# Kernel tuning notes

Hardware: AMD Instinct MI355X
Metric: run time of the kernel (lower is better)

## Reference

```python
import jax, jax.numpy as jnp
import numpy as np

B, S, H = 4, 4096, 2048


def setup_inputs() -> dict:
    key = jax.random.key(0)
    ks = jax.random.split(key, 20)
    def lin(k, fin, fout):
        # torch nn.Linear default init: U(-1/sqrt(fin), 1/sqrt(fin))
        kw, kb = jax.random.split(k)
        bound = 1.0 / np.sqrt(fin)
        W = jax.random.uniform(kw, (fin, fout), jnp.float32, -bound, bound)
        b = jax.random.uniform(kb, (fout,), jnp.float32, -bound, bound)
        return W, b
    hidden_states = jax.random.normal(ks[0], (B, S, H), jnp.float32)
    access_frequency = jax.random.uniform(ks[1], (B, S), jnp.float32)
    importance_score = jax.random.uniform(ks[2], (B, S), jnp.float32)
    sel_W1, sel_b1 = lin(ks[3], H, H // 4)
    sel_W2, sel_b2 = lin(ks[4], H // 4, 3)
    c1_W, c1_b = lin(ks[5], H, H // 2)
    f1_W, f1_b = lin(ks[6], H // 2, H // 2)
    d1_W, d1_b = lin(ks[7], H // 2, H)
    c2_W, c2_b = lin(ks[8], H, H // 4)
    f2_W, f2_b = lin(ks[9], H // 4, H // 4)
    d2_W, d2_b = lin(ks[10], H // 4, H)
    return dict(hidden_states=hidden_states, access_frequency=access_frequency,
                importance_score=importance_score, sel_W1=sel_W1, sel_b1=sel_b1,
                sel_W2=sel_W2, sel_b2=sel_b2, c1_W=c1_W, c1_b=c1_b, f1_W=f1_W,
                f1_b=f1_b, d1_W=d1_W, d1_b=d1_b, c2_W=c2_W, c2_b=c2_b,
                f2_W=f2_W, f2_b=f2_b, d2_W=d2_W, d2_b=d2_b)


def reference(hidden_states, access_frequency, importance_score,
              sel_W1, sel_b1, sel_W2, sel_b2,
              c1_W, c1_b, f1_W, f1_b, d1_W, d1_b,
              c2_W, c2_b, f2_W, f2_b, d2_W, d2_b):
    x = hidden_states  # [B,S,H]
    Hh = x.shape[-1] // 2
    # strategy selector on frequency/importance-modulated features
    combined = jnp.concatenate(
        [x[..., :Hh] * access_frequency[..., None],
         x[..., Hh:] * importance_score[..., None]], axis=-1)  # [B,S,H]
    hmid = jax.nn.relu(jnp.einsum('bsh,hk->bsk', combined, sel_W1) + sel_b1)
    weights = jax.nn.softmax(jnp.einsum('bsk,kl->bsl', hmid, sel_W2) + sel_b2)
    sel = jnp.argmax(weights, axis=-1)  # [B,S] in {0,1,2}
    # expert paths (computed densely, selected per token)
    out1 = (jax.numpy.einsum('bsh,hc->bsc', x, c1_W) + c1_b)
    out1 = jnp.einsum('bsc,cd->bsd', out1, f1_W) + f1_b
    out1 = jnp.einsum('bsc,ch->bsh', out1, d1_W) + d1_b
    out2 = (jnp.einsum('bsh,hc->bsc', x, c2_W) + c2_b)
    out2 = jnp.einsum('bsc,cd->bsd', out2, f2_W) + f2_b
    out2 = jnp.einsum('bsc,ch->bsh', out2, d2_W) + d2_b
    s = sel[..., None]
    out = jnp.where(s == 0, x, jnp.where(s == 1, out1, out2))
    return out
```

## Files before the change

kernel.cpp:

```cpp
#include <hip/hip_runtime.h>


typedef __bf16 bf16x8 __attribute__((ext_vector_type(8)));
typedef float  f32x4  __attribute__((ext_vector_type(4)));
typedef unsigned short us;

__device__ __forceinline__ float bf2f(us u) {
  union { unsigned u; float f; } v; v.u = ((unsigned)u) << 16;
  return v.f;
}
__device__ __forceinline__ us f2bf(float f) {
  union { float f; unsigned u; } v; v.f = f;
  unsigned r = v.u + 0x7fffu + ((v.u >> 16) & 1u);
  return (us)(r >> 16);
}
__device__ __forceinline__ float scrub(float v) {
  return (v == v && fabsf(v) < 1e30f) ? v : 0.f;
}
__device__ __forceinline__ void gld_lds16(const void* g, void* l) {
  __builtin_amdgcn_global_load_lds(
      (const __attribute__((address_space(1))) void*)g,
      (__attribute__((address_space(3))) void*)l, 16, 0, 0);
}

template<int MODE, int AIDX>
__global__ __launch_bounds__(256) void gemm_bt(
    const void* __restrict__ Ap, const us* __restrict__ BT,
    const float* __restrict__ bias, void* __restrict__ outp,
    const int* __restrict__ aidx, const int* __restrict__ oidx,
    const int* __restrict__ cntp, int N, int K)
{
  const int cnt = cntp[0];
  const int Mp  = (cnt + 127) & ~127;
  const int bm0 = blockIdx.y * 128;
  if (bm0 >= Mp) return;
  const int bn0 = blockIdx.x * 128;

  __shared__ __align__(16) us As[128 * 64];
  __shared__ __align__(16) us Bs[128 * 64];
  const int tid  = threadIdx.x;
  const int lane = tid & 63;
  const int w    = tid >> 6;
  const int wr   = w >> 1, wc = w & 1;

  const us* gb[4];
  const us* gab[4];
  const float* gaf[4];
  us* la[4]; us* lb[4];
#pragma unroll
  for (int i = 0; i < 4; ++i) {
    const int s = i * 256 + tid, m = s >> 3, cp = s & 7, c = cp ^ (m & 7);
    gb[i] = BT + (size_t)(bn0 + m) * K + c * 8;
    lb[i] = &Bs[s * 8];
    la[i] = &As[s * 8];
    if (AIDX) {
      const int arow = aidx[bm0 + m];
      gaf[i] = (const float*)Ap + (size_t)arow * K + c * 8;
    } else {
      gab[i] = (const us*)Ap + (size_t)(bm0 + m) * K + c * 8;
    }
  }

  f32x4 acc[4][4] = {};

  for (int k0 = 0; k0 < K; k0 += 64) {
#pragma unroll
    for (int i = 0; i < 4; ++i) { gld_lds16(gb[i], lb[i]); gb[i] += 64; }
    if (AIDX) {
#pragma unroll
      for (int i = 0; i < 4; ++i) {
        float4 a0 = *(const float4*)gaf[i];
        float4 a1 = *(const float4*)(gaf[i] + 4);
        gaf[i] += 64;
        union { uint4 v; us u[8]; } t;
        t.u[0] = f2bf(a0.x); t.u[1] = f2bf(a0.y);
        t.u[2] = f2bf(a0.z); t.u[3] = f2bf(a0.w);
        t.u[4] = f2bf(a1.x); t.u[5] = f2bf(a1.y);
        t.u[6] = f2bf(a1.z); t.u[7] = f2bf(a1.w);
        *(uint4*)la[i] = t.v;
      }
    } else {
#pragma unroll
      for (int i = 0; i < 4; ++i) { gld_lds16(gab[i], la[i]); gab[i] += 64; }
    }
    __syncthreads();
#pragma unroll
    for (int kk = 0; kk < 2; ++kk) {
      const int cc = kk * 4 + (lane >> 4);
      bf16x8 af[4], bfr[4];
#pragma unroll
      for (int t = 0; t < 4; ++t) {
        const int m = wr * 64 + t * 16 + (lane & 15);
        const int n = wc * 64 + t * 16 + (lane & 15);
        af[t]  = *(const bf16x8*)&As[(m * 8 + (cc ^ (m & 7))) * 8];
        bfr[t] = *(const bf16x8*)&Bs[(n * 8 + (cc ^ (n & 7))) * 8];
      }
#pragma unroll
      for (int mt = 0; mt < 4; ++mt)
#pragma unroll
        for (int nt = 0; nt < 4; ++nt)
          acc[mt][nt] = __builtin_amdgcn_mfma_f32_16x16x32_bf16(
              af[mt], bfr[nt], acc[mt][nt], 0, 0, 0);
    }
    __syncthreads();
  }

  const int colb = bn0 + wc * 64 + (lane & 15);
  const int rowb = bm0 + wr * 64 + ((lane >> 4) << 2);
  float bv[4];
#pragma unroll
  for (int nt = 0; nt < 4; ++nt) bv[nt] = bias[colb + nt * 16];
#pragma unroll
  for (int mt = 0; mt < 4; ++mt) {
#pragma unroll
    for (int r = 0; r < 4; ++r) {
      const int row = rowb + mt * 16 + r;
      if (MODE == 3) {
        if (row >= cnt) continue;
        const size_t orow = (size_t)oidx[row];
#pragma unroll
        for (int nt = 0; nt < 4; ++nt)
          ((float*)outp)[orow * N + colb + nt * 16] =
              scrub(acc[mt][nt][r] + bv[nt]);
      } else {
#pragma unroll
        for (int nt = 0; nt < 4; ++nt)
          ((us*)outp)[(size_t)row * N + colb + nt * 16] =
              f2bf(scrub(acc[mt][nt][r] + bv[nt]));
      }
    }
  }
}

__global__ __launch_bounds__(256) void sel_gemm(
    const float* __restrict__ X, const float* __restrict__ FR,
    const float* __restrict__ IM,
    const us* __restrict__ BTH, const us* __restrict__ BTL,
    const float* __restrict__ bias, float* __restrict__ hmid)
{
  constexpr int K = 2048, N = 512;
  __shared__ __align__(16) us AsH[128 * 64];
  __shared__ __align__(16) us AsL[128 * 64];
  __shared__ __align__(16) us BsH[128 * 64];
  __shared__ __align__(16) us BsL[128 * 64];
  const int tid  = threadIdx.x;
  const int lane = tid & 63;
  const int w    = tid >> 6;
  const int wr   = w >> 1, wc = w & 1;
  const int bm0  = blockIdx.y * 128;
  const int bn0  = blockIdx.x * 128;

  const us* gbh[4]; const us* gbl[4];
  const float* gx[4];
  us* lbh[4]; us* lbl[4];
  int sOfs[4];
#pragma unroll
  for (int i = 0; i < 4; ++i) {
    const int s = i * 256 + tid, m = s >> 3, cp = s & 7, c = cp ^ (m & 7);
    gbh[i] = BTH + (size_t)(bn0 + m) * K + c * 8;
    gbl[i] = BTL + (size_t)(bn0 + m) * K + c * 8;
    lbh[i] = &BsH[s * 8];
    lbl[i] = &BsL[s * 8];
    gx[i]  = X + (size_t)(bm0 + m) * K + c * 8;
    sOfs[i] = s * 8;
  }

  f32x4 acc[4][4] = {};

  for (int k0 = 0; k0 < K; k0 += 64) {
#pragma unroll
    for (int i = 0; i < 4; ++i) {
      gld_lds16(gbh[i], lbh[i]); gbh[i] += 64;
      gld_lds16(gbl[i], lbl[i]); gbl[i] += 64;
    }
#pragma unroll
    for (int i = 0; i < 4; ++i) {
      const int s = i * 256 + tid, m = s >> 3, cp = s & 7, c = cp ^ (m & 7);
      const float md = (k0 + c * 8 < 1024) ? FR[bm0 + m] : IM[bm0 + m];
      float4 a0 = *(const float4*)gx[i];
      float4 a1 = *(const float4*)(gx[i] + 4);
      gx[i] += 64;
      float av[8] = {a0.x, a0.y, a0.z, a0.w, a1.x, a1.y, a1.z, a1.w};
      union { uint4 v; us u[8]; } hu, lu;
#pragma unroll
      for (int j = 0; j < 8; ++j) {
        float a = av[j] * md;
        us h = f2bf(a);
        hu.u[j] = h;
        lu.u[j] = f2bf(a - bf2f(h));
      }
      *(uint4*)&AsH[sOfs[i]] = hu.v;
      *(uint4*)&AsL[sOfs[i]] = lu.v;
    }
    __syncthreads();
#pragma unroll
    for (int kk = 0; kk < 2; ++kk) {
      const int cc = kk * 4 + (lane >> 4);
      bf16x8 ah[4], al[4], bh[4], bl[4];
#pragma unroll
      for (int t = 0; t < 4; ++t) {
        const int m = wr * 64 + t * 16 + (lane & 15);
        const int n = wc * 64 + t * 16 + (lane & 15);
        const int ai = (m * 8 + (cc ^ (m & 7))) * 8;
        const int bi = (n * 8 + (cc ^ (n & 7))) * 8;
        ah[t] = *(const bf16x8*)&AsH[ai];
        al[t] = *(const bf16x8*)&AsL[ai];
        bh[t] = *(const bf16x8*)&BsH[bi];
        bl[t] = *(const bf16x8*)&BsL[bi];
      }
#pragma unroll
      for (int mt = 0; mt < 4; ++mt)
#pragma unroll
        for (int nt = 0; nt < 4; ++nt) {
          acc[mt][nt] = __builtin_amdgcn_mfma_f32_16x16x32_bf16(
              ah[mt], bh[nt], acc[mt][nt], 0, 0, 0);
          acc[mt][nt] = __builtin_amdgcn_mfma_f32_16x16x32_bf16(
              al[mt], bh[nt], acc[mt][nt], 0, 0, 0);
          acc[mt][nt] = __builtin_amdgcn_mfma_f32_16x16x32_bf16(
              ah[mt], bl[nt], acc[mt][nt], 0, 0, 0);
        }
    }
    __syncthreads();
  }

  const int colb = bn0 + wc * 64 + (lane & 15);
  const int rowb = bm0 + wr * 64 + ((lane >> 4) << 2);
  float bv[4];
#pragma unroll
  for (int nt = 0; nt < 4; ++nt) bv[nt] = bias[colb + nt * 16];
#pragma unroll
  for (int mt = 0; mt < 4; ++mt)
#pragma unroll
    for (int r = 0; r < 4; ++r) {
      const int row = rowb + mt * 16 + r;
#pragma unroll
      for (int nt = 0; nt < 4; ++nt)
        hmid[(size_t)row * N + colb + nt * 16] =
            fmaxf(scrub(acc[mt][nt][r] + bv[nt]), 0.f);
    }
}

__global__ __launch_bounds__(256) void logits_argmax(
    const float* __restrict__ hmid, const float* __restrict__ W2,
    const float* __restrict__ B2, int* __restrict__ sel)
{
  const int lane = threadIdx.x & 63;
  const int wv   = threadIdx.x >> 6;
  const int t    = blockIdx.x * 4 + wv;
  const float* h = hmid + (size_t)t * 512;
  double s0 = 0.0, s1 = 0.0, s2 = 0.0;
#pragma unroll
  for (int j = 0; j < 8; ++j) {
    int e = j * 64 + lane;
    double hv = (double)h[e];
    s0 += hv * (double)W2[e * 3 + 0];
    s1 += hv * (double)W2[e * 3 + 1];
    s2 += hv * (double)W2[e * 3 + 2];
  }
  for (int o = 32; o > 0; o >>= 1) {
    s0 += __shfl_down(s0, o);
    s1 += __shfl_down(s1, o);
    s2 += __shfl_down(s2, o);
  }
  if (lane == 0) {
    s0 += (double)B2[0]; s1 += (double)B2[1]; s2 += (double)B2[2];
    int idx = 0; double b = s0;
    if (s1 > b) { b = s1; idx = 1; }
    if (s2 > b) { idx = 2; }
    sel[t] = idx;
  }
}

__global__ __launch_bounds__(256) void compact(
    const int* __restrict__ sel, int* __restrict__ cnt,
    int* __restrict__ idx1, int* __restrict__ idx2)
{
  const int t    = blockIdx.x * 256 + threadIdx.x;
  const int lane = threadIdx.x & 63;
  const int w    = threadIdx.x >> 6;
  const int s    = sel[t];
  const bool f1 = (s == 1), f2 = (s == 2);
  const unsigned long long m1 = __ballot(f1);
  const unsigned long long m2 = __ballot(f2);
  const unsigned long long lt = (1ull << lane) - 1ull;
  const int b1 = __popcll(m1 & lt);
  const int b2 = __popcll(m2 & lt);
  __shared__ int w1[4], w2[4], base1, base2;
  if (lane == 0) { w1[w] = __popcll(m1); w2[w] = __popcll(m2); }
  __syncthreads();
  if (threadIdx.x == 0) {
    base1 = atomicAdd(&cnt[0], w1[0] + w1[1] + w1[2] + w1[3]);
    base2 = atomicAdd(&cnt[1], w2[0] + w2[1] + w2[2] + w2[3]);
  }
  __syncthreads();
  int o1 = base1, o2 = base2;
  for (int i = 0; i < w; ++i) { o1 += w1[i]; o2 += w2[i]; }
  if (f1) idx1[o1 + b1] = t;
  if (f2) idx2[o2 + b2] = t;
}

__global__ __launch_bounds__(128) void pad_idx(
    const int* __restrict__ cnt, int* __restrict__ idx1, int* __restrict__ idx2)
{
  idx1[cnt[0] + threadIdx.x] = 0;
  idx2[cnt[1] + threadIdx.x] = 0;
}

__global__ __launch_bounds__(256) void pass0(
    const float* __restrict__ X, const int* __restrict__ sel,
    float* __restrict__ OUT)
{
  const int t = blockIdx.x;
  if (sel[t] != 0) return;
  const uint4* src = (const uint4*)(X + (size_t)t * 2048);
  uint4* dst = (uint4*)(OUT + (size_t)t * 2048);
  dst[threadIdx.x]       = src[threadIdx.x];
  dst[threadIdx.x + 256] = src[threadIdx.x + 256];
}

__global__ __launch_bounds__(256) void transpose_f2b(
    const float* __restrict__ W, us* __restrict__ WT, int K, int N)
{
  __shared__ float tile[32][33];
  const int tx = threadIdx.x & 31, ty = threadIdx.x >> 5;
  const int n0 = blockIdx.x * 32, k0 = blockIdx.y * 32;
#pragma unroll
  for (int r = 0; r < 4; ++r)
    tile[ty + r * 8][tx] = W[(size_t)(k0 + ty + r * 8) * N + n0 + tx];
  __syncthreads();
#pragma unroll
  for (int r = 0; r < 4; ++r)
    WT[(size_t)(n0 + ty + r * 8) * K + k0 + tx] = f2bf(tile[tx][ty + r * 8]);
}

__global__ __launch_bounds__(256) void transpose_split(
    const float* __restrict__ W, us* __restrict__ WH, us* __restrict__ WL,
    int K, int N)
{
  __shared__ float tile[32][33];
  const int tx = threadIdx.x & 31, ty = threadIdx.x >> 5;
  const int n0 = blockIdx.x * 32, k0 = blockIdx.y * 32;
#pragma unroll
  for (int r = 0; r < 4; ++r)
    tile[ty + r * 8][tx] = W[(size_t)(k0 + ty + r * 8) * N + n0 + tx];
  __syncthreads();
#pragma unroll
  for (int r = 0; r < 4; ++r) {
    float v = tile[tx][ty + r * 8];
    us h = f2bf(v);
    const size_t o = (size_t)(n0 + ty + r * 8) * K + k0 + tx;
    WH[o] = h;
    WL[o] = f2bf(v - bf2f(h));
  }
}

extern "C" void kernel_launch(void* const* d_in, const int* in_sizes, int n_in,
                              void* d_out, int out_size, void* d_ws, size_t ws_size,
                              hipStream_t stream) {
  const float* X   = (const float*)d_in[0];
  const float* FR  = (const float*)d_in[1];
  const float* IM  = (const float*)d_in[2];
  const float* W1  = (const float*)d_in[3];
  const float* B1  = (const float*)d_in[4];
  const float* W2  = (const float*)d_in[5];
  const float* B2  = (const float*)d_in[6];
  const float* C1W = (const float*)d_in[7];
  const float* C1B = (const float*)d_in[8];
  const float* F1W = (const float*)d_in[9];
  const float* F1B = (const float*)d_in[10];
  const float* D1W = (const float*)d_in[11];
  const float* D1B = (const float*)d_in[12];
  const float* C2W = (const float*)d_in[13];
  const float* C2B = (const float*)d_in[14];
  const float* F2W = (const float*)d_in[15];
  const float* F2B = (const float*)d_in[16];
  const float* D2W = (const float*)d_in[17];
  const float* D2B = (const float*)d_in[18];
  float* OUT = (float*)d_out;

  size_t off = 0;
  auto alloc = [&](size_t bytes) -> void* {
    void* p = (char*)d_ws + off;
    off += (bytes + 255) & ~(size_t)255;
    return p;
  };
  us* WT_selH = (us*)alloc(512ull * 2048 * 2);
  us* WT_selL = (us*)alloc(512ull * 2048 * 2);
  us* WT_c1   = (us*)alloc(1024ull * 2048 * 2);
  us* WT_f1   = (us*)alloc(1024ull * 1024 * 2);
  us* WT_d1   = (us*)alloc(2048ull * 1024 * 2);
  us* WT_c2   = (us*)alloc(512ull * 2048 * 2);
  us* WT_f2   = (us*)alloc(512ull * 512 * 2);
  us* WT_d2   = (us*)alloc(2048ull * 512 * 2);
  int* sel    = (int*)alloc(16384ull * 4);
  int* cnt    = (int*)alloc(2 * 4);
  int* idx1   = (int*)alloc((16384ull + 128) * 4);
  int* idx2   = (int*)alloc((16384ull + 128) * 4);
  void* R1    = alloc(16384ull * 1024 * 2);
  void* R2    = alloc(16384ull * 1024 * 2);
  if (ws_size < off) return;

  float* hmid = (float*)R1;
  us* t1 = (us*)R1;
  us* u1 = (us*)R1;
  us* t2 = (us*)R2;
  us* u2 = (us*)R2;

  const dim3 blk(256);
  transpose_split<<<dim3(16, 64), blk, 0, stream>>>(W1, WT_selH, WT_selL, 2048, 512);
  transpose_f2b<<<dim3(32, 64), blk, 0, stream>>>(C1W, WT_c1, 2048, 1024);
  transpose_f2b<<<dim3(32, 32), blk, 0, stream>>>(F1W, WT_f1, 1024, 1024);
  transpose_f2b<<<dim3(64, 32), blk, 0, stream>>>(D1W, WT_d1, 1024, 2048);
  transpose_f2b<<<dim3(16, 64), blk, 0, stream>>>(C2W, WT_c2, 2048, 512);
  transpose_f2b<<<dim3(16, 16), blk, 0, stream>>>(F2W, WT_f2, 512, 512);
  transpose_f2b<<<dim3(64, 16), blk, 0, stream>>>(D2W, WT_d2, 512, 2048);

  sel_gemm<<<dim3(4, 128), blk, 0, stream>>>(X, FR, IM, WT_selH, WT_selL, B1, hmid);
  logits_argmax<<<dim3(4096), blk, 0, stream>>>(hmid, W2, B2, sel);
  hipMemsetAsync(cnt, 0, 8, stream);
  compact<<<dim3(64), blk, 0, stream>>>(sel, cnt, idx1, idx2);
  pad_idx<<<dim3(1), dim3(128), 0, stream>>>(cnt, idx1, idx2);

  pass0<<<dim3(16384), blk, 0, stream>>>(X, sel, OUT);

  gemm_bt<0, 1><<<dim3(8, 128), blk, 0, stream>>>(X,  WT_c1, C1B, t1, idx1, nullptr, cnt + 0, 1024, 2048);
  gemm_bt<0, 0><<<dim3(8, 128), blk, 0, stream>>>(t1, WT_f1, F1B, t2, nullptr, nullptr, cnt + 0, 1024, 1024);
  gemm_bt<3, 0><<<dim3(16, 128), blk, 0, stream>>>(t2, WT_d1, D1B, OUT, nullptr, idx1, cnt + 0, 2048, 1024);

  gemm_bt<0, 1><<<dim3(4, 128), blk, 0, stream>>>(X,  WT_c2, C2B, u1, idx2, nullptr, cnt + 1, 512, 2048);
  gemm_bt<0, 0><<<dim3(4, 128), blk, 0, stream>>>(u1, WT_f2, F2B, u2, nullptr, nullptr, cnt + 1, 512, 512);
  gemm_bt<3, 0><<<dim3(16, 128), blk, 0, stream>>>(u2, WT_d2, D2B, OUT, nullptr, idx2, cnt + 1, 2048, 512);
}
```

Measured before the change: 643.1 us.

## Run selector GEMM in single bf16, recompute near-tie tokens with split precision

The selector GEMM now runs once in plain bf16, with no hi/lo split of activations and weights, which cuts its MFMA and LDS work roughly to a quarter. Tokens whose top-two logits lie within a small margin are collected into an index list. Only those tokens are recomputed with the original split-bf16 GEMM, and their argmax is overwritten. This adds extra launches and an atomic compaction step, and correctness depends on the margin covering the bf16 error.

```diff
diff --git a/kernel.cpp b/kernel.cpp
--- a/kernel.cpp
+++ b/kernel.cpp
@@ -1,5 +1,7 @@
 #include <hip/hip_runtime.h>
 
+
+#define RECHECK_TAU 0.02
 
 typedef __bf16 bf16x8 __attribute__((ext_vector_type(8)));
 typedef float  f32x4  __attribute__((ext_vector_type(4)));
@@ -132,13 +134,106 @@
   }
 }
 
-__global__ __launch_bounds__(256) void sel_gemm(
+__global__ __launch_bounds__(256) void sel_fast(
+    const float* __restrict__ X, const float* __restrict__ FR,
+    const float* __restrict__ IM, const us* __restrict__ BTH,
+    const float* __restrict__ bias, float* __restrict__ hmid)
+{
+  constexpr int K = 2048, N = 512;
+  __shared__ __align__(16) us As[128 * 64];
+  __shared__ __align__(16) us Bs[128 * 64];
+  const int tid  = threadIdx.x;
+  const int lane = tid & 63;
+  const int w    = tid >> 6;
+  const int wr   = w >> 1, wc = w & 1;
+  const int bm0  = blockIdx.y * 128;
+  const int bn0  = blockIdx.x * 128;
+
+  const us* gb[4]; const float* gx[4]; us* lb[4];
+  int sOfs[4], cth[4];
+  float fr[4], im[4];
+#pragma unroll
+  for (int i = 0; i < 4; ++i) {
+    const int s = i * 256 + tid, m = s >> 3, cp = s & 7, c = cp ^ (m & 7);
+    gb[i] = BTH + (size_t)(bn0 + m) * K + c * 8;
+    lb[i] = &Bs[s * 8];
+    gx[i] = X + (size_t)(bm0 + m) * K + c * 8;
+    sOfs[i] = s * 8;
+    cth[i]  = c * 8;
+    fr[i] = FR[bm0 + m];
+    im[i] = IM[bm0 + m];
+  }
+
+  f32x4 acc[4][4] = {};
+
+  for (int k0 = 0; k0 < K; k0 += 64) {
+#pragma unroll
+    for (int i = 0; i < 4; ++i) { gld_lds16(gb[i], lb[i]); gb[i] += 64; }
+#pragma unroll
+    for (int i = 0; i < 4; ++i) {
+      const float md = (k0 + cth[i] < 1024) ? fr[i] : im[i];
+      float4 a0 = *(const float4*)gx[i];
+      float4 a1 = *(const float4*)(gx[i] + 4);
+      gx[i] += 64;
+      float av[8] = {a0.x, a0.y, a0.z, a0.w, a1.x, a1.y, a1.z, a1.w};
+      union { uint4 v; us u[8]; } t;
+#pragma unroll
+      for (int j = 0; j < 8; ++j) t.u[j] = f2bf(av[j] * md);
+      *(uint4*)&As[sOfs[i]] = t.v;
+    }
+    __syncthreads();
+#pragma unroll
+    for (int kk = 0; kk < 2; ++kk) {
+      const int cc = kk * 4 + (lane >> 4);
+      bf16x8 af[4], bfr[4];
+#pragma unroll
+      for (int t = 0; t < 4; ++t) {
+        const int m = wr * 64 + t * 16 + (lane & 15);
+        const int n = wc * 64 + t * 16 + (lane & 15);
+        af[t]  = *(const bf16x8*)&As[(m * 8 + (cc ^ (m & 7))) * 8];
+        bfr[t] = *(const bf16x8*)&Bs[(n * 8 + (cc ^ (n & 7))) * 8];
+      }
+#pragma unroll
+      for (int mt = 0; mt < 4; ++mt)
+#pragma unroll
+        for (int nt = 0; nt < 4; ++nt)
+          acc[mt][nt] = __builtin_amdgcn_mfma_f32_16x16x32_bf16(
+              af[mt], bfr[nt], acc[mt][nt], 0, 0, 0);
+    }
+    __syncthreads();
+  }
+
+  const int colb = bn0 + wc * 64 + (lane & 15);
+  const int rowb = bm0 + wr * 64 + ((lane >> 4) << 2);
+  float bv[4];
+#pragma unroll
+  for (int nt = 0; nt < 4; ++nt) bv[nt] = bias[colb + nt * 16];
+#pragma unroll
+  for (int mt = 0; mt < 4; ++mt)
+#pragma unroll
+    for (int r = 0; r < 4; ++r) {
+      const int row = rowb + mt * 16 + r;
+#pragma unroll
+      for (int nt = 0; nt < 4; ++nt)
+        hmid[(size_t)row * N + colb + nt * 16] =
+            fmaxf(scrub(acc[mt][nt][r] + bv[nt]), 0.f);
+    }
+}
+
+__global__ __launch_bounds__(256) void sel_precise(
     const float* __restrict__ X, const float* __restrict__ FR,
     const float* __restrict__ IM,
     const us* __restrict__ BTH, const us* __restrict__ BTL,
-    const float* __restrict__ bias, float* __restrict__ hmid)
+    const float* __restrict__ bias, float* __restrict__ hmid_r,
+    const int* __restrict__ ridx, const int* __restrict__ cntp)
 {
   constexpr int K = 2048, N = 512;
+  const int cnt = cntp[0];
+  const int Mp  = (cnt + 127) & ~127;
+  const int bm0 = blockIdx.y * 128;
+  if (bm0 >= Mp) return;
+  const int bn0 = blockIdx.x * 128;
+
   __shared__ __align__(16) us AsH[128 * 64];
   __shared__ __align__(16) us AsL[128 * 64];
   __shared__ __align__(16) us BsH[128 * 64];
@@ -147,13 +242,12 @@
   const int lane = tid & 63;
   const int w    = tid >> 6;
   const int wr   = w >> 1, wc = w & 1;
-  const int bm0  = blockIdx.y * 128;
-  const int bn0  = blockIdx.x * 128;
 
   const us* gbh[4]; const us* gbl[4];
   const float* gx[4];
   us* lbh[4]; us* lbl[4];
-  int sOfs[4];
+  int sOfs[4], cth[4];
+  float fr[4], im[4];
 #pragma unroll
   for (int i = 0; i < 4; ++i) {
     const int s = i * 256 + tid, m = s >> 3, cp = s & 7, c = cp ^ (m & 7);
@@ -161,8 +255,12 @@
     gbl[i] = BTL + (size_t)(bn0 + m) * K + c * 8;
     lbh[i] = &BsH[s * 8];
     lbl[i] = &BsL[s * 8];
-    gx[i]  = X + (size_t)(bm0 + m) * K + c * 8;
+    const int arow = ridx[bm0 + m];
+    gx[i]  = X + (size_t)arow * K + c * 8;
     sOfs[i] = s * 8;
+    cth[i]  = c * 8;
+    fr[i] = FR[arow];
+    im[i] = IM[arow];
   }
 
   f32x4 acc[4][4] = {};
@@ -175,8 +273,7 @@
     }
 #pragma unroll
     for (int i = 0; i < 4; ++i) {
-      const int s = i * 256 + tid, m = s >> 3, cp = s & 7, c = cp ^ (m & 7);
-      const float md = (k0 + c * 8 < 1024) ? FR[bm0 + m] : IM[bm0 + m];
+      const float md = (k0 + cth[i] < 1024) ? fr[i] : im[i];
       float4 a0 = *(const float4*)gx[i];
       float4 a1 = *(const float4*)(gx[i] + 4);
       gx[i] += 64;
@@ -235,14 +332,15 @@
       const int row = rowb + mt * 16 + r;
 #pragma unroll
       for (int nt = 0; nt < 4; ++nt)
-        hmid[(size_t)row * N + colb + nt * 16] =
+        hmid_r[(size_t)row * N + colb + nt * 16] =
             fmaxf(scrub(acc[mt][nt][r] + bv[nt]), 0.f);
     }
 }
 
-__global__ __launch_bounds__(256) void logits_argmax(
+__global__ __launch_bounds__(256) void logits_gap(
     const float* __restrict__ hmid, const float* __restrict__ W2,
-    const float* __restrict__ B2, int* __restrict__ sel)
+    const float* __restrict__ B2, int* __restrict__ sel,
+    int* __restrict__ cntr, int* __restrict__ ridx)
 {
   const int lane = threadIdx.x & 63;
   const int wv   = threadIdx.x >> 6;
@@ -266,8 +364,47 @@
     s0 += (double)B2[0]; s1 += (double)B2[1]; s2 += (double)B2[2];
     int idx = 0; double b = s0;
     if (s1 > b) { b = s1; idx = 1; }
+    if (s2 > b) { b = s2; idx = 2; }
+    sel[t] = idx;
+    const double mn = fmin(fmin(s0, s1), s2);
+    const double second = (s0 + s1 + s2) - b - mn;
+    if (b - second < RECHECK_TAU) {
+      const int p = atomicAdd(cntr, 1);
+      ridx[p] = t;
+    }
+  }
+}
+
+__global__ __launch_bounds__(256) void logits_fix(
+    const float* __restrict__ hmid_r, const float* __restrict__ W2,
+    const float* __restrict__ B2, const int* __restrict__ cntr,
+    const int* __restrict__ ridx, int* __restrict__ sel)
+{
+  const int lane = threadIdx.x & 63;
+  const int wv   = threadIdx.x >> 6;
+  const int r    = blockIdx.x * 4 + wv;
+  if (r >= cntr[0]) return;
+  const float* h = hmid_r + (size_t)r * 512;
+  double s0 = 0.0, s1 = 0.0, s2 = 0.0;
+#pragma unroll
+  for (int j = 0; j < 8; ++j) {
+    int e = j * 64 + lane;
+    double hv = (double)h[e];
+    s0 += hv * (double)W2[e * 3 + 0];
+    s1 += hv * (double)W2[e * 3 + 1];
+    s2 += hv * (double)W2[e * 3 + 2];
+  }
+  for (int o = 32; o > 0; o >>= 1) {
+    s0 += __shfl_down(s0, o);
+    s1 += __shfl_down(s1, o);
+    s2 += __shfl_down(s2, o);
+  }
+  if (lane == 0) {
+    s0 += (double)B2[0]; s1 += (double)B2[1]; s2 += (double)B2[2];
+    int idx = 0; double b = s0;
+    if (s1 > b) { b = s1; idx = 1; }
     if (s2 > b) { idx = 2; }
-    sel[t] = idx;
+    sel[ridx[r]] = idx;
   }
 }
 
@@ -304,6 +441,12 @@
 {
   idx1[cnt[0] + threadIdx.x] = 0;
   idx2[cnt[1] + threadIdx.x] = 0;
+}
+
+__global__ __launch_bounds__(128) void pad_r(
+    const int* __restrict__ cntr, int* __restrict__ ridx)
+{
+  ridx[cntr[0] + threadIdx.x] = 0;
 }
 
 __global__ __launch_bounds__(256) void pass0(
@@ -393,14 +536,16 @@
   us* WT_f2   = (us*)alloc(512ull * 512 * 2);
   us* WT_d2   = (us*)alloc(2048ull * 512 * 2);
   int* sel    = (int*)alloc(16384ull * 4);
-  int* cnt    = (int*)alloc(2 * 4);
+  int* cnt    = (int*)alloc(3 * 4);
   int* idx1   = (int*)alloc((16384ull + 128) * 4);
   int* idx2   = (int*)alloc((16384ull + 128) * 4);
+  int* ridx   = (int*)alloc((16384ull + 128) * 4);
   void* R1    = alloc(16384ull * 1024 * 2);
   void* R2    = alloc(16384ull * 1024 * 2);
   if (ws_size < off) return;
 
-  float* hmid = (float*)R1;
+  float* hmid   = (float*)R1;
+  float* hmid_r = (float*)R2;
   us* t1 = (us*)R1;
   us* u1 = (us*)R1;
   us* t2 = (us*)R2;
@@ -415,9 +560,16 @@
   transpose_f2b<<<dim3(16, 16), blk, 0, stream>>>(F2W, WT_f2, 512, 512);
   transpose_f2b<<<dim3(64, 16), blk, 0, stream>>>(D2W, WT_d2, 512, 2048);
 
-  sel_gemm<<<dim3(4, 128), blk, 0, stream>>>(X, FR, IM, WT_selH, WT_selL, B1, hmid);
-  logits_argmax<<<dim3(4096), blk, 0, stream>>>(hmid, W2, B2, sel);
-  hipMemsetAsync(cnt, 0, 8, stream);
+  hipMemsetAsync(cnt, 0, 12, stream);
+
+  sel_fast<<<dim3(4, 128), blk, 0, stream>>>(X, FR, IM, WT_selH, B1, hmid);
+  logits_gap<<<dim3(4096), blk, 0, stream>>>(hmid, W2, B2, sel, cnt + 2, ridx);
+  pad_r<<<dim3(1), dim3(128), 0, stream>>>(cnt + 2, ridx);
+
+  sel_precise<<<dim3(4, 128), blk, 0, stream>>>(X, FR, IM, WT_selH, WT_selL,
+                                                B1, hmid_r, ridx, cnt + 2);
+  logits_fix<<<dim3(4096), blk, 0, stream>>>(hmid_r, W2, B2, cnt + 2, ridx, sel);
+
   compact<<<dim3(64), blk, 0, stream>>>(sel, cnt, idx1, idx2);
   pad_idx<<<dim3(1), dim3(128), 0, stream>>>(cnt, idx1, idx2);
 
```

Measured after the change: 747.5 us. 1.16x slower.
